# Optimization experiments

Hardware: AMD Instinct MI355X
Metric: run time of the kernel (lower is better)

## Reference

```python
import jax, jax.numpy as jnp
import numpy as np

EPS = 1e-8
LN_EPS = 1e-5
DIM, NHEADS = 512, 8
HEAD_DIM = DIM // NHEADS
SCALE = HEAD_DIM ** -0.5
ROLE_VOCAB = 8


def _layernorm(x, g, b):
    mu = x.mean(-1, keepdims=True)
    var = ((x - mu) ** 2).mean(-1, keepdims=True)
    return (x - mu) * jax.lax.rsqrt(var + LN_EPS) * g + b


def setup_inputs() -> dict:
    key = jax.random.key(0)
    ks = jax.random.split(key, 16)
    B, K, L, D = 8, 4, 1024, DIM
    s = 1.0 / np.sqrt(D)
    return {
        "state_repr": jax.random.normal(ks[0], (B, K, L, D), jnp.float32),
        "residue_mask": jax.random.randint(ks[1], (B, K, L), 0, 2) > 0,
        "state_weights": jax.random.uniform(ks[2], (B, K), jnp.float32),
        "state_roles": jax.random.randint(ks[3], (B, K), 0, ROLE_VOCAB),
        "state_present_mask": jnp.ones((B, K), dtype=bool),
        "role_emb": jax.random.normal(ks[4], (ROLE_VOCAB, D), jnp.float32),
        "Wq": jax.random.normal(ks[5], (D, D), jnp.float32) * s,
        "Wk": jax.random.normal(ks[6], (D, D), jnp.float32) * s,
        "Wv": jax.random.normal(ks[7], (D, D), jnp.float32) * s,
        "Wo": jax.random.normal(ks[8], (D, D), jnp.float32) * s,
        "ln1_g": jnp.ones((3 * D,), jnp.float32),
        "ln1_b": jnp.zeros((3 * D,), jnp.float32),
        "Wg1": jax.random.normal(ks[9], (D, 3 * D), jnp.float32) / np.sqrt(3 * D),
        "bg1": jnp.zeros((D,), jnp.float32),
        "Wg2": jax.random.normal(ks[10], (D, D), jnp.float32) * s,
        "bg2": jnp.zeros((D,), jnp.float32),
        "norm_g": jnp.ones((D,), jnp.float32),
        "norm_b": jnp.zeros((D,), jnp.float32),
    }


def _forward(state_repr, residue_mask, state_weights, state_roles, state_present_mask,
             role_emb, Wq, Wk, Wv, Wo, ln1_g, ln1_b, Wg1, bg1, Wg2, bg2, norm_g, norm_b):
    B, K, L, D = state_repr.shape
    H, hd = NHEADS, HEAD_DIM
    roles = jnp.maximum(state_roles, 0)
    role_e = role_emb[roles][:, :, None, :]                       # [B,K,1,D]
    valid = residue_mask & state_present_mask[:, :, None]          # [B,K,L]

    # normalized state weights
    pres = state_present_mask.astype(jnp.float32)
    w = state_weights.astype(jnp.float32) * pres
    denom = w.sum(1, keepdims=True)
    fallback = pres / jnp.maximum(pres.sum(1, keepdims=True), 1.0)
    nsw = jnp.where(denom > EPS, w / jnp.maximum(denom, EPS), fallback)  # [B,K]

    x = (state_repr + role_e) * valid[..., None]
    x = x.transpose(0, 2, 1, 3)                                    # [B,L,K,D]
    valid_rlk = valid.transpose(0, 2, 1)                           # [B,L,K]

    def proj(W):  # torch Linear: y = x @ W.T
        return (x @ W.T).reshape(B, L, K, H, hd).transpose(0, 1, 3, 2, 4)  # [B,L,H,K,hd]

    q, k, v = proj(Wq), proj(Wk), proj(Wv)
    logits = jnp.einsum('blhqd,blhkd->blhqk', q, k) * SCALE
    logits = logits + jnp.log(jnp.maximum(nsw, EPS))[:, None, None, None, :]
    key_mask = valid_rlk[:, :, None, None, :]                      # [B,L,1,1,K]
    logits = jnp.where(key_mask, logits, -jnp.inf)
    attn = jax.nn.softmax(logits, axis=-1)
    attn = jnp.nan_to_num(attn, nan=0.0, posinf=0.0, neginf=0.0)
    attn_out = jnp.einsum('blhqk,blhkd->blhqd', attn, v)
    attn_out = attn_out.transpose(0, 1, 3, 2, 4).reshape(B, L, K, D)
    attn_out = (attn_out @ Wo.T) * valid_rlk[..., None]

    swr = nsw[:, None, :] * valid_rlk.astype(jnp.float32)          # [B,L,K]
    swr = swr / jnp.maximum(swr.sum(-1, keepdims=True), EPS)
    weighted_mean = jnp.sum(x * swr[..., None], axis=2)            # [B,L,D]
    attn_pooled = jnp.sum(attn_out * swr[..., None], axis=2)

    max_in = jnp.where(valid_rlk[..., None], x, -1e9)
    max_feat = max_in.max(axis=2)
    has_any = valid_rlk.any(axis=2, keepdims=True)
    max_feat = jnp.where(has_any, max_feat, 0.0)

    fusion_base = 0.5 * (attn_pooled + weighted_mean)
    gate_in = jnp.concatenate([attn_pooled, weighted_mean, max_feat], axis=-1)
    h = _layernorm(gate_in, ln1_g, ln1_b)
    h = jax.nn.gelu(h @ Wg1.T + bg1, approximate=False)
    gate = jax.nn.sigmoid(h @ Wg2.T + bg2)
    fused = gate * fusion_base + (1.0 - gate) * max_feat
    fused = _layernorm(fused + weighted_mean, norm_g, norm_b)

    attn_mean = attn.mean(axis=(2, 3))                             # [B,L,K]
    return fused, attn_pooled, weighted_mean, max_feat, attn_mean, nsw


def reference(state_repr, residue_mask, state_weights, state_roles, state_present_mask,
              role_emb, Wq, Wk, Wv, Wo, ln1_g, ln1_b, Wg1, bg1, Wg2, bg2, norm_g, norm_b):
    return _forward(state_repr, residue_mask, state_weights, state_roles, state_present_mask,
                    role_emb, Wq, Wk, Wv, Wo, ln1_g, ln1_b, Wg1, bg1, Wg2, bg2, norm_g, norm_b)
```

## Files before the change

kernel.cpp:

```cpp
#include <hip/hip_runtime.h>
#include <math.h>

#define BB 8
#define KK 4
#define LL 1024
#define DD 512
#define HD 64
#define D3 1536
#define MM (BB*LL*KK)
#define BL (BB*LL)
#define SCALE 0.125f
#define EPSF 1e-8f
#define LN_EPSF 1e-5f

typedef _Float16 hfrag __attribute__((ext_vector_type(8)));
typedef float f32x4 __attribute__((ext_vector_type(4)));

__device__ __forceinline__ unsigned short f2h(float f) {
    _Float16 h = (_Float16)f;
    unsigned short u; __builtin_memcpy(&u, &h, 2); return u;
}
__device__ __forceinline__ float h2f(unsigned short u) {
    _Float16 h; __builtin_memcpy(&h, &u, 2); return (float)h;
}

__device__ __forceinline__ void glds16(const unsigned short* g, unsigned short* l) {
    __builtin_amdgcn_global_load_lds(
        (const __attribute__((address_space(1))) void*)g,
        (__attribute__((address_space(3))) void*)l, 16, 0, 0);
}

__device__ __forceinline__ void nsw_compute(const float* sw, const int* pres,
                                            int b, float* nswv) {
    float w[KK], pr[KK]; float denom = 0.f, ps = 0.f;
    #pragma unroll
    for (int k = 0; k < KK; ++k) {
        pr[k] = pres[b*KK + k] ? 1.f : 0.f;
        w[k]  = sw[b*KK + k] * pr[k];
        denom += w[k]; ps += pr[k];
    }
    #pragma unroll
    for (int k = 0; k < KK; ++k)
        nswv[k] = (denom > EPSF) ? w[k] / fmaxf(denom, EPSF)
                                 : pr[k] / fmaxf(ps, 1.f);
}

#define WSZ 262144
#define OG1 1048576
#define OG2 1835008
#define WTOT 2097152
__global__ __launch_bounds__(256) void cvt_weights(
        const float* __restrict__ Wq, const float* __restrict__ Wk,
        const float* __restrict__ Wv, const float* __restrict__ Wo,
        const float* __restrict__ Wg1, const float* __restrict__ Wg2,
        unsigned short* __restrict__ dst) {
    int t = blockIdx.x * 256 + threadIdx.x;
    int e = t * 4;
    const float* src; int off;
    if      (e < WSZ)    { src = Wq;  off = e; }
    else if (e < 2*WSZ)  { src = Wk;  off = e - WSZ; }
    else if (e < 3*WSZ)  { src = Wv;  off = e - 2*WSZ; }
    else if (e < OG1)    { src = Wo;  off = e - 3*WSZ; }
    else if (e < OG2)    { src = Wg1; off = e - OG1; }
    else                 { src = Wg2; off = e - OG2; }
    float4 v = *(const float4*)(src + off);
    ushort4 o;
    o.x = f2h(v.x); o.y = f2h(v.y); o.z = f2h(v.z); o.w = f2h(v.w);
    *(ushort4*)(dst + e) = o;
}

__global__ __launch_bounds__(256) void buildx_kernel(
        const float* __restrict__ SR, const int* __restrict__ residue,
        const int* __restrict__ pres, const int* __restrict__ roles,
        const float* __restrict__ role_emb, const float* __restrict__ sw,
        unsigned short* __restrict__ Xh, float* __restrict__ rowmask,
        float* __restrict__ out_wm, float* __restrict__ out_mx,
        float* __restrict__ f_nsw) {
    int t  = blockIdx.x * 256 + threadIdx.x;
    int bl = t >> 7;
    int d4 = (t & 127) << 2;
    int b  = bl >> 10, l = bl & 1023;
    float nswv[KK];
    nsw_compute(sw, pres, b, nswv);
    float mk[KK], swr[KK];
    float ssum = 0.f, many = 0.f;
    #pragma unroll
    for (int k = 0; k < KK; ++k) {
        int bk = b*KK + k;
        bool valid = (residue[(size_t)bk*LL + l] != 0) && (pres[bk] != 0);
        mk[k]  = valid ? 1.f : 0.f;
        swr[k] = nswv[k] * mk[k];
        ssum += swr[k]; many += mk[k];
    }
    float inv = 1.f / fmaxf(ssum, EPSF);
    bool hasany = many > 0.5f;
    float wmx = 0.f, wmy = 0.f, wmz = 0.f, wmw = 0.f;
    float mxx = -1e9f, mxy = -1e9f, mxz = -1e9f, mxw = -1e9f;
    #pragma unroll
    for (int k = 0; k < KK; ++k) {
        int bk = b*KK + k;
        int role = roles[bk]; if (role < 0) role = 0;
        float4 sr = *(const float4*)(SR + ((size_t)bk*LL + l)*DD + d4);
        float4 re = *(const float4*)(role_emb + (size_t)role*DD + d4);
        float xx = (sr.x + re.x)*mk[k], xy = (sr.y + re.y)*mk[k];
        float xz = (sr.z + re.z)*mk[k], xw = (sr.w + re.w)*mk[k];
        ushort4 xs; xs.x = f2h(xx); xs.y = f2h(xy); xs.z = f2h(xz); xs.w = f2h(xw);
        *(ushort4*)(Xh + (size_t)(bl*KK + k)*DD + d4) = xs;
        float s = swr[k]*inv;
        wmx = fmaf(xx, s, wmx); wmy = fmaf(xy, s, wmy);
        wmz = fmaf(xz, s, wmz); wmw = fmaf(xw, s, wmw);
        if (mk[k] > 0.5f) {
            mxx = fmaxf(mxx, xx); mxy = fmaxf(mxy, xy);
            mxz = fmaxf(mxz, xz); mxw = fmaxf(mxw, xw);
        }
    }
    if (!hasany) { mxx = mxy = mxz = mxw = 0.f; }
    float4 wmv; wmv.x = wmx; wmv.y = wmy; wmv.z = wmz; wmv.w = wmw;
    float4 mxv; mxv.x = mxx; mxv.y = mxy; mxv.z = mxz; mxv.w = mxw;
    *(float4*)(out_wm + (size_t)bl*DD + d4) = wmv;
    *(float4*)(out_mx + (size_t)bl*DD + d4) = mxv;
    if (d4 == 0) {
        #pragma unroll
        for (int k = 0; k < KK; ++k) rowmask[bl*KK + k] = mk[k];
    }
    if (blockIdx.x == 0 && threadIdx.x < BB*KK) {
        int bb = threadIdx.x >> 2, kk2 = threadIdx.x & 3;
        float nv[KK];
        nsw_compute(sw, pres, bb, nv);
        f_nsw[threadIdx.x] = nv[kk2];
    }
}

template<int TM, int EPI, int OUTH, int QKVR, int SWZ>
__global__ __launch_bounds__(256) void gemm_mfma(
        const unsigned short* __restrict__ A, const unsigned short* __restrict__ W,
        void* __restrict__ Cv, int M, int N, int Kd,
        const float* __restrict__ bias, const float* __restrict__ rowmask) {
    constexpr int FI = TM / 32;
    __shared__ __align__(16) unsigned short As[TM*32];
    __shared__ __align__(16) unsigned short Bs[128*32];
    const int tid  = threadIdx.x;
    const int wave = tid >> 6, lane = tid & 63;
    int m0, n0;
    if (SWZ) {
        int id = blockIdx.x;
        int c = id & 7, j = id >> 3;
        int mloc = j / 12;
        m0 = (c*32 + mloc) * TM;
        n0 = (j - mloc*12) * 128;
    } else {
        m0 = blockIdx.y * TM; n0 = blockIdx.x * 128;
    }
    const int srow = lane >> 2;
    const int scol = (lane & 3) << 3;
    const int arow = (TM == 128) ? (wave*32 + srow)
                   : (TM == 64)  ? (wave*16 + srow)
                   :               ((wave & 1)*16 + srow);
    const bool astage = (TM >= 64) || (wave < 2);
    const unsigned short* Ag0 = A + (size_t)(m0 + arow) * Kd + scol;
    const unsigned short* Ag1 = Ag0 + (size_t)16 * Kd;
    unsigned short* Al0 = As + arow*32 + scol;
    unsigned short* Al1 = Al0 + 16*32;
    const unsigned short* Wp0 = W + (size_t)(n0 + wave*32 + srow) * Kd + scol;
    const unsigned short* Wp1 = Wp0 + (size_t)16 * Kd;
    unsigned short* Bl0 = Bs + (wave*32 + srow)*32 + scol;
    unsigned short* Bl1 = Bl0 + 16*32;
    const int wr = (wave >> 1) * (TM/2);
    const int wc = (wave & 1) * 64;
    const int fr = lane & 15;
    const int fq = (lane >> 4) * 8;
    f32x4 acc[FI][4] = {};
    for (int k0 = 0; k0 < Kd; k0 += 32) {
        if (astage)    glds16(Ag0 + k0, Al0);
        if (TM == 128) glds16(Ag1 + k0, Al1);
        glds16(Wp0 + k0, Bl0);
        glds16(Wp1 + k0, Bl1);
        __syncthreads();
        hfrag af[FI], bf[4];
        #pragma unroll
        for (int i = 0; i < FI; ++i)
            af[i] = *(const hfrag*)(As + (wr + i*16 + fr)*32 + fq);
        #pragma unroll
        for (int j = 0; j < 4; ++j)
            bf[j] = *(const hfrag*)(Bs + (wc + j*16 + fr)*32 + fq);
        #pragma unroll
        for (int i = 0; i < FI; ++i)
            #pragma unroll
            for (int j = 0; j < 4; ++j)
                acc[i][j] = __builtin_amdgcn_mfma_f32_16x16x32_f16(af[i], bf[j], acc[i][j], 0, 0, 0);
        __syncthreads();
    }
    unsigned short* Ch = (unsigned short*)Cv;
    int Nout = N, colbase = n0;
    if (QKVR) {
        const int seg = n0 >> 9;
        Ch = (unsigned short*)Cv + (size_t)seg * M * 512;
        Nout = 512;
        colbase = n0 - (seg << 9);
    }
    #pragma unroll
    for (int i = 0; i < FI; ++i) {
        const int row = m0 + wr + i*16 + (lane >> 4)*4;
        #pragma unroll
        for (int j = 0; j < 4; ++j) {
            const int col = colbase + wc + j*16 + (lane & 15);
            float bv = (EPI == 2) ? bias[col] : 0.f;
            #pragma unroll
            for (int r = 0; r < 4; ++r) {
                float v = acc[i][j][r];
                if (EPI == 2) { v += bv; v = 0.5f * v * (1.f + erff(v * 0.70710678118654752f)); }
                if (OUTH) Ch[(size_t)(row + r) * Nout + col] = f2h(v);
                else      ((float*)Cv)[(size_t)(row + r) * Nout + col] = v;
            }
        }
    }
}

__global__ __launch_bounds__(512, 4) void gemm_qkv_8p(
        const unsigned short* __restrict__ A, const unsigned short* __restrict__ W,
        unsigned short* __restrict__ Cbase) {
    __shared__ __align__(16) unsigned short smem[36864];
    const int tid  = threadIdx.x;
    const int wave = tid >> 6, lane = tid & 63;
    const int id = blockIdx.x;
    const int wg = (id & 7) * 192 + (id >> 3);
    const int m0 = (wg / 12) * 256;
    const int n0 = (wg % 12) * 128;
    const int wm = wave >> 1, wn = wave & 1;
    const int fr = lane & 15, q = lane >> 4;
    const int srow = tid >> 2, scc = tid & 3;
    const int sswz = (scc ^ ((srow >> 1) & 3)) << 3;
    const unsigned short* Ag0 = A + (size_t)(m0 + srow)*512 + sswz;
    const unsigned short* Ag1 = Ag0 + (size_t)128*512;
    const unsigned short* Wg0 = W + (size_t)(n0 + srow)*512 + sswz;
    const int lA0 = tid << 3;
    const int lA1 = (tid + 512) << 3;
    int aoff[4], boff[4];
    #pragma unroll
    for (int mf = 0; mf < 4; ++mf) {
        int row = (wm << 6) + (mf << 4) + fr;
        aoff[mf] = (row << 5) + ((q ^ ((row >> 1) & 3)) << 3);
    }
    #pragma unroll
    for (int nf = 0; nf < 4; ++nf) {
        int row = (wn << 6) + (nf << 4) + fr;
        boff[nf] = (row << 5) + ((q ^ ((row >> 1) & 3)) << 3);
    }
    f32x4 acc[4][4] = {};

#define VMWAIT(N) asm volatile("s_waitcnt vmcnt(" #N ")" ::: "memory")
#define STAGE(tt) do { unsigned short* _d = smem + ((tt) % 3) * 12288; \
        const int _ko = (tt) << 5; \
        glds16(Ag0 + _ko, _d + lA0); glds16(Ag1 + _ko, _d + lA1); \
        glds16(Wg0 + _ko, _d + 8192 + lA0); } while (0)
#define MFROW(ai, areg) \
        acc[ai][0] = __builtin_amdgcn_mfma_f32_16x16x32_f16(areg, b0, acc[ai][0], 0, 0, 0); \
        acc[ai][1] = __builtin_amdgcn_mfma_f32_16x16x32_f16(areg, b1, acc[ai][1], 0, 0, 0); \
        acc[ai][2] = __builtin_amdgcn_mfma_f32_16x16x32_f16(areg, b2, acc[ai][2], 0, 0, 0); \
        acc[ai][3] = __builtin_amdgcn_mfma_f32_16x16x32_f16(areg, b3, acc[ai][3], 0, 0, 0);
#define TILE(t, STG, VM) do { \
        const unsigned short* _Ab = smem + ((t) % 3) * 12288; \
        const unsigned short* _Bb = _Ab + 8192; \
        VMWAIT(VM); \
        __builtin_amdgcn_s_barrier(); \
        __builtin_amdgcn_sched_barrier(0); \
        hfrag b0 = *(const hfrag*)(_Bb + boff[0]); \
        hfrag b1 = *(const hfrag*)(_Bb + boff[1]); \
        hfrag b2 = *(const hfrag*)(_Bb + boff[2]); \
        hfrag b3 = *(const hfrag*)(_Bb + boff[3]); \
        hfrag a0_ = *(const hfrag*)(_Ab + aoff[0]); \
        hfrag a1_ = *(const hfrag*)(_Ab + aoff[1]); \
        hfrag a2_ = *(const hfrag*)(_Ab + aoff[2]); \
        hfrag a3_ = *(const hfrag*)(_Ab + aoff[3]); \
        if (STG) STAGE((t) + 2); \
        __builtin_amdgcn_s_setprio(1); \
        MFROW(0, a0_) MFROW(1, a1_) MFROW(2, a2_) MFROW(3, a3_) \
        __builtin_amdgcn_s_setprio(0); \
    } while (0)

    STAGE(0); STAGE(1);
    #pragma unroll
    for (int t = 0; t < 14; ++t) TILE(t, 1, 3);
    TILE(14, 0, 3);
    TILE(15, 0, 0);
#undef TILE
#undef MFROW
#undef STAGE
#undef VMWAIT

    const int gc0 = n0 + (wn << 6);
    const int seg = gc0 >> 9;
    unsigned short* Cs = Cbase + (size_t)seg * ((size_t)MM * 512);
    const int cb = gc0 & 511;
    #pragma unroll
    for (int mf = 0; mf < 4; ++mf) {
        const int grow = m0 + (wm << 6) + (mf << 4) + (q << 2);
        #pragma unroll
        for (int nf = 0; nf < 4; ++nf) {
            const int col = cb + (nf << 4) + fr;
            #pragma unroll
            for (int r = 0; r < 4; ++r)
                Cs[(size_t)(grow + r) * 512 + col] = f2h(acc[mf][nf][r]);
        }
    }
}

__global__ __launch_bounds__(256) void wo_pool_kernel(
        const unsigned short* __restrict__ A,
        const unsigned short* __restrict__ W,
        const float* __restrict__ sw, const int* __restrict__ pres,
        const float* __restrict__ rmask,
        const float* __restrict__ in_wm, const float* __restrict__ in_mx,
        const float* __restrict__ ln1_g, const float* __restrict__ ln1_b,
        float* __restrict__ out_ap, unsigned short* __restrict__ hin) {
    __shared__ __align__(16) unsigned short As[32*32];
    __shared__ __align__(16) unsigned short Bs[512*32];
    const int tid = threadIdx.x, wave = tid >> 6, lane = tid & 63;
    const int m0 = blockIdx.x * 32;
    const int srow = lane >> 2, scol = (lane & 3) << 3;
    const unsigned short* Ag = A + (size_t)(m0 + wave*16 + srow)*512 + scol;
    unsigned short* Al = As + (wave*16 + srow)*32 + scol;
    const int brow = wave*128 + srow;
    const unsigned short* Wg = W + (size_t)brow*512 + scol;
    unsigned short* Blb = Bs + brow*32 + scol;
    const int q = lane >> 4, frl = lane & 15;
    const int fq = q * 8;
    f32x4 acc[2][8] = {};
    for (int k0 = 0; k0 < 512; k0 += 32) {
        if (wave < 2) glds16(Ag + k0, Al);
        #pragma unroll
        for (int i = 0; i < 8; ++i)
            glds16(Wg + (size_t)i*16*512 + k0, Blb + i*16*32);
        __syncthreads();
        hfrag af[2], bf[8];
        #pragma unroll
        for (int i = 0; i < 2; ++i)
            af[i] = *(const hfrag*)(As + (i*16 + frl)*32 + fq);
        #pragma unroll
        for (int j = 0; j < 8; ++j)
            bf[j] = *(const hfrag*)(Bs + (wave*128 + j*16 + frl)*32 + fq);
        #pragma unroll
        for (int i = 0; i < 2; ++i)
            #pragma unroll
            for (int j = 0; j < 8; ++j)
                acc[i][j] = __builtin_amdgcn_mfma_f32_16x16x32_f16(af[i], bf[j], acc[i][j], 0, 0, 0);
        __syncthreads();
    }
    float* ap_s = (float*)Bs;
    const int bl0 = m0 >> 2;
    const int b = bl0 >> 10;
    float nv[KK];
    nsw_compute(sw, pres, b, nv);
    #pragma unroll
    for (int i = 0; i < 2; ++i) {
        int bl_loc = i*4 + q;
        int blg = bl0 + bl_loc;
        float s4[KK]; float ssum = 0.f;
        #pragma unroll
        for (int k = 0; k < KK; ++k) { s4[k] = nv[k] * rmask[blg*4 + k]; ssum += s4[k]; }
        float inv = 1.f / fmaxf(ssum, EPSF);
        #pragma unroll
        for (int j = 0; j < 8; ++j) {
            float ap = 0.f;
            #pragma unroll
            for (int r = 0; r < KK; ++r) ap = fmaf(s4[r]*inv, acc[i][j][r], ap);
            ap_s[bl_loc*512 + wave*128 + j*16 + frl] = ap;
        }
    }
    __syncthreads();
    const int blq = tid >> 5;
    const int c0  = (tid & 31) * 16;
    const int blg = bl0 + blq;
    float4 ap4[4], wm4[4], mx4[4];
    #pragma unroll
    for (int v = 0; v < 4; ++v) {
        ap4[v] = *(const float4*)(ap_s + blq*512 + c0 + v*4);
        wm4[v] = *(const float4*)(in_wm + (size_t)blg*512 + c0 + v*4);
        mx4[v] = *(const float4*)(in_mx + (size_t)blg*512 + c0 + v*4);
    }
    float s = 0.f, s2 = 0.f;
    #pragma unroll
    for (int c = 0; c < 16; ++c) {
        float ap = ((const float*)ap4)[c];
        float wm = ((const float*)wm4)[c];
        float mx = ((const float*)mx4)[c];
        s += ap + wm + mx; s2 += ap*ap + wm*wm + mx*mx;
    }
    #pragma unroll
    for (int o = 1; o < 32; o <<= 1) {
        s  += __shfl_xor(s,  o, 32);
        s2 += __shfl_xor(s2, o, 32);
    }
    float mu = s * (1.f/(float)D3);
    float var = s2 * (1.f/(float)D3) - mu*mu;
    float rstd = rsqrtf(var + LN_EPSF);
    #pragma unroll
    for (int v = 0; v < 4; ++v)
        *(float4*)(out_ap + (size_t)blg*512 + c0 + v*4) = ap4[v];
    #pragma unroll
    for (int seg = 0; seg < 3; ++seg) {
        const float* src = (seg == 0) ? (const float*)ap4
                         : (seg == 1) ? (const float*)wm4 : (const float*)mx4;
        int gofs = seg*512 + c0;
        #pragma unroll
        for (int v = 0; v < 4; ++v) {
            float4 g4 = *(const float4*)(ln1_g + gofs + v*4);
            float4 b4 = *(const float4*)(ln1_b + gofs + v*4);
            ushort4 o;
            o.x = f2h((src[v*4+0]-mu)*rstd*g4.x + b4.x);
            o.y = f2h((src[v*4+1]-mu)*rstd*g4.y + b4.y);
            o.z = f2h((src[v*4+2]-mu)*rstd*g4.z + b4.z);
            o.w = f2h((src[v*4+3]-mu)*rstd*g4.w + b4.w);
            *(ushort4*)(hin + (size_t)blg*D3 + gofs + v*4) = o;
        }
    }
}

__global__ __launch_bounds__(256) void wg2_final_kernel(
        const unsigned short* __restrict__ A,
        const unsigned short* __restrict__ W,
        const float* __restrict__ bg2,
        const float* __restrict__ in_ap, const float* __restrict__ in_wm,
        const float* __restrict__ in_mx,
        const float* __restrict__ norm_g, const float* __restrict__ norm_b,
        float* __restrict__ fused) {
    __shared__ __align__(16) unsigned short As[16*32];
    __shared__ __align__(16) unsigned short Bs[512*32];
    __shared__ float rs[16*4], rq[16*4];
    const int tid = threadIdx.x, wave = tid >> 6, lane = tid & 63;
    const int m0 = blockIdx.x * 16;
    const int srow = lane >> 2, scol = (lane & 3) << 3;
    const unsigned short* Ag = A + (size_t)(m0 + srow)*512 + scol;
    unsigned short* Al = As + srow*32 + scol;
    const int brow = wave*128 + srow;
    const unsigned short* Wg = W + (size_t)brow*512 + scol;
    unsigned short* Blb = Bs + brow*32 + scol;
    const int q = lane >> 4, frl = lane & 15;
    const int fq = q * 8;
    f32x4 acc[8] = {};
    for (int k0 = 0; k0 < 512; k0 += 32) {
        if (wave == 0) glds16(Ag + k0, Al);
        #pragma unroll
        for (int i = 0; i < 8; ++i)
            glds16(Wg + (size_t)i*16*512 + k0, Blb + i*16*32);
        __syncthreads();
        hfrag af, bf[8];
        af = *(const hfrag*)(As + frl*32 + fq);
        #pragma unroll
        for (int j = 0; j < 8; ++j)
            bf[j] = *(const hfrag*)(Bs + (wave*128 + j*16 + frl)*32 + fq);
        #pragma unroll
        for (int j = 0; j < 8; ++j)
            acc[j] = __builtin_amdgcn_mfma_f32_16x16x32_f16(af, bf[j], acc[j], 0, 0, 0);
        __syncthreads();
    }
    float pre[8][4];
    float s[4] = {}, s2[4] = {};
    #pragma unroll
    for (int j = 0; j < 8; ++j) {
        int col = wave*128 + j*16 + frl;
        float bv = bg2[col];
        #pragma unroll
        for (int r = 0; r < 4; ++r) {
            int row = m0 + q*4 + r;
            float g = 1.f / (1.f + expf(-(acc[j][r] + bv)));
            float ap = in_ap[(size_t)row*512 + col];
            float wm = in_wm[(size_t)row*512 + col];
            float mx = in_mx[(size_t)row*512 + col];
            float p = g*0.5f*(ap + wm) + (1.f - g)*mx + wm;
            pre[j][r] = p;
            s[r] += p; s2[r] += p*p;
        }
    }
    #pragma unroll
    for (int r = 0; r < 4; ++r) {
        #pragma unroll
        for (int o = 1; o < 16; o <<= 1) {
            s[r]  += __shfl_xor(s[r],  o, 64);
            s2[r] += __shfl_xor(s2[r], o, 64);
        }
        if (frl == 0) {
            rs[(q*4+r)*4 + wave] = s[r];
            rq[(q*4+r)*4 + wave] = s2[r];
        }
    }
    __syncthreads();
    float mu[4], rstd[4];
    #pragma unroll
    for (int r = 0; r < 4; ++r) {
        int rl = q*4 + r;
        float ts  = rs[rl*4] + rs[rl*4+1] + rs[rl*4+2] + rs[rl*4+3];
        float tq  = rq[rl*4] + rq[rl*4+1] + rq[rl*4+2] + rq[rl*4+3];
        float m = ts * (1.f/(float)DD);
        float v = tq * (1.f/(float)DD) - m*m;
        mu[r] = m; rstd[r] = rsqrtf(v + LN_EPSF);
    }
    #pragma unroll
    for (int j = 0; j < 8; ++j) {
        int col = wave*128 + j*16 + frl;
        float g = norm_g[col], bb = norm_b[col];
        #pragma unroll
        for (int r = 0; r < 4; ++r) {
            int row = m0 + q*4 + r;
            fused[(size_t)row*512 + col] = (pre[j][r]-mu[r])*rstd[r]*g + bb;
        }
    }
}

__global__ __launch_bounds__(256) void attn_kernel(
        unsigned short* Qb ,
        const unsigned short* __restrict__ Kb, const unsigned short* __restrict__ Vb,
        const float* __restrict__ sw, const int* __restrict__ pres,
        const float* __restrict__ rowmask,
        float* __restrict__ attn_mean_out) {
    __shared__ float qs[KK][DD];
    __shared__ float ksm[KK][DD];
    __shared__ float vs[KK][DD];
    __shared__ float att[128];
    __shared__ float lw[KK], mk[KK];
    int bl = blockIdx.x, b = bl >> 10, mb = bl * KK;
    int tid = threadIdx.x;
    const ushort4* q4 = (const ushort4*)(Qb + (size_t)mb*DD);
    const ushort4* k4 = (const ushort4*)(Kb + (size_t)mb*DD);
    const ushort4* v4 = (const ushort4*)(Vb + (size_t)mb*DD);
    #pragma unroll
    for (int p = 0; p < 2; ++p) {
        int idx = p*256 + tid;
        int k = idx >> 7, dd = (idx & 127) << 2;
        ushort4 a = q4[idx];
        qs[k][dd] = h2f(a.x); qs[k][dd+1] = h2f(a.y); qs[k][dd+2] = h2f(a.z); qs[k][dd+3] = h2f(a.w);
        ushort4 c = k4[idx];
        ksm[k][dd] = h2f(c.x); ksm[k][dd+1] = h2f(c.y); ksm[k][dd+2] = h2f(c.z); ksm[k][dd+3] = h2f(c.w);
        ushort4 e = v4[idx];
        vs[k][dd] = h2f(e.x); vs[k][dd+1] = h2f(e.y); vs[k][dd+2] = h2f(e.z); vs[k][dd+3] = h2f(e.w);
    }
    if (tid < KK) {
        float nv[KK];
        nsw_compute(sw, pres, b, nv);
        lw[tid] = logf(fmaxf(nv[tid], EPSF));
        mk[tid] = rowmask[mb + tid];
    }
    __syncthreads();
    if (tid < 128) {
        int h = tid >> 4, i = (tid >> 2) & 3, j = tid & 3;
        float s = 0.f;
        #pragma unroll 16
        for (int d = 0; d < HD; ++d) s = fmaf(qs[i][h*HD + d], ksm[j][h*HD + d], s);
        float lg = s * SCALE + lw[j];
        att[tid] = (mk[j] > 0.5f) ? lg : -INFINITY;
    }
    __syncthreads();
    if (tid < 32) {
        int base = tid * 4;
        float l0 = att[base], l1 = att[base+1], l2 = att[base+2], l3 = att[base+3];
        float m = fmaxf(fmaxf(l0, l1), fmaxf(l2, l3));
        if (m == -INFINITY) {
            att[base] = att[base+1] = att[base+2] = att[base+3] = 0.f;
        } else {
            float e0 = expf(l0 - m), e1 = expf(l1 - m), e2 = expf(l2 - m), e3 = expf(l3 - m);
            float inv = 1.f / (e0 + e1 + e2 + e3);
            att[base] = e0*inv; att[base+1] = e1*inv; att[base+2] = e2*inv; att[base+3] = e3*inv;
        }
    }
    __syncthreads();
    if (tid < KK) {
        float s = 0.f;
        for (int hi = 0; hi < 32; ++hi) s += att[hi*4 + tid];
        attn_mean_out[(size_t)bl*KK + tid] = s * (1.f/32.f);
    }
    float outv[8];
    #pragma unroll
    for (int p = 0; p < 8; ++p) {
        int idx = p*256 + tid;
        int i = idx >> 9, dc = idx & 511, h = dc >> 6;
        float s = 0.f;
        #pragma unroll
        for (int j = 0; j < KK; ++j) s = fmaf(att[h*16 + i*4 + j], vs[j][dc], s);
        outv[p] = s;
    }
    #pragma unroll
    for (int p = 0; p < 8; ++p) {
        int idx = p*256 + tid;
        int i = idx >> 9, dc = idx & 511;
        Qb[(size_t)(mb+i)*DD + dc] = f2h(outv[p]);
    }
}

extern "C" void kernel_launch(void* const* d_in, const int* in_sizes, int n_in,
                              void* d_out, int out_size, void* d_ws, size_t ws_size,
                              hipStream_t stream) {
    const float* SR      = (const float*)d_in[0];
    const int*   residue = (const int*)d_in[1];
    const float* sw      = (const float*)d_in[2];
    const int*   roles   = (const int*)d_in[3];
    const int*   pres    = (const int*)d_in[4];
    const float* role_emb= (const float*)d_in[5];
    const float* Wq      = (const float*)d_in[6];
    const float* Wk      = (const float*)d_in[7];
    const float* Wv      = (const float*)d_in[8];
    const float* Wo      = (const float*)d_in[9];
    const float* ln1_g   = (const float*)d_in[10];
    const float* ln1_b   = (const float*)d_in[11];
    const float* Wg1     = (const float*)d_in[12];
    const float* bg1     = (const float*)d_in[13];
    const float* Wg2     = (const float*)d_in[14];
    const float* bg2     = (const float*)d_in[15];
    const float* norm_g  = (const float*)d_in[16];
    const float* norm_b  = (const float*)d_in[17];

    float* out = (float*)d_out;
    const size_t BLD = (size_t)BL * DD;
    float* f_fused = out;
    float* f_ap    = out + BLD;
    float* f_wm    = out + 2*BLD;
    float* f_mx    = out + 3*BLD;
    float* f_am    = out + 4*BLD;
    float* f_nsw   = out + 4*BLD + (size_t)BL*KK;

    char* base = (char*)d_ws;
    const size_t MD2 = (size_t)MM * DD * 2;
    unsigned short* Xh = (unsigned short*)(base);
    unsigned short* Qh = (unsigned short*)(base + MD2);
    unsigned short* Kh = (unsigned short*)(base + 2*MD2);
    unsigned short* Vh = (unsigned short*)(base + 3*MD2);
    unsigned short* Wb = (unsigned short*)(base + 4*MD2);
    float* rmask = (float*)(base + 4*MD2 + (size_t)WTOT*2);
    unsigned short* AOh  = Qh;
    unsigned short* Hin  = Vh;
    unsigned short* Hbuf = Xh;
    const unsigned short* Wqkv = Wb;
    const unsigned short* Woh  = Wb + 3*WSZ;
    const unsigned short* Wg1h = Wb + OG1;
    const unsigned short* Wg2h = Wb + OG2;

    dim3 blk(256);

    cvt_weights<<<WTOT/1024, blk, 0, stream>>>(Wq, Wk, Wv, Wo, Wg1, Wg2, Wb);
    buildx_kernel<<<(BL*128)/256, blk, 0, stream>>>(SR, residue, pres, roles, role_emb,
                                                    sw, Xh, rmask, f_wm, f_mx, f_nsw);

    gemm_qkv_8p<<<dim3(1536), dim3(512), 0, stream>>>(Xh, Wqkv, Qh);

    attn_kernel<<<BL, blk, 0, stream>>>(Qh, Kh, Vh, sw, pres, rmask, f_am);

    wo_pool_kernel<<<dim3(MM/32), blk, 0, stream>>>(
        AOh, Woh, sw, pres, rmask, f_wm, f_mx, ln1_g, ln1_b, f_ap, Hin);

    gemm_mfma<32,2,1,0,0><<<dim3(4, BL/32), blk, 0, stream>>>(
        Hin, Wg1h, Hbuf, BL, DD, D3, bg1, nullptr);

    wg2_final_kernel<<<dim3(BL/16), blk, 0, stream>>>(
        Hbuf, Wg2h, bg2, f_ap, f_wm, f_mx, norm_g, norm_b, f_fused);
}
```

Baseline: 375.2 us.

## Replace gate GEMM with triple-buffered swizzled MFMA kernel; stream attention from global

Swaps the generic 32-row gate-1 GEMM for a dedicated 128x128-tile kernel. It uses triple-buffered async global-to-LDS staging, XOR-swizzled LDS layout, explicit vmcnt waits and priority hints, with the bias+GELU epilogue fused in. Separately, the attention kernel drops its LDS staging of Q/K/V in fp32. It now reads Q/K as 16-byte half vectors directly from global memory for the scores and V as half2 pairs for the output, which removes LDS traffic and occupancy pressure. The GEMM change trades tile size and grid width (256 blocks) for better reuse and latency hiding. The attention change relies on cache hits for repeated global reads.

Result: faster. 353.7 us (-5.7%).

```diff
diff --git a/kernel.cpp b/kernel.cpp
--- a/kernel.cpp
+++ b/kernel.cpp
@@ -128,91 +128,6 @@
         float nv[KK];
         nsw_compute(sw, pres, bb, nv);
         f_nsw[threadIdx.x] = nv[kk2];
-    }
-}
-
-template<int TM, int EPI, int OUTH, int QKVR, int SWZ>
-__global__ __launch_bounds__(256) void gemm_mfma(
-        const unsigned short* __restrict__ A, const unsigned short* __restrict__ W,
-        void* __restrict__ Cv, int M, int N, int Kd,
-        const float* __restrict__ bias, const float* __restrict__ rowmask) {
-    constexpr int FI = TM / 32;
-    __shared__ __align__(16) unsigned short As[TM*32];
-    __shared__ __align__(16) unsigned short Bs[128*32];
-    const int tid  = threadIdx.x;
-    const int wave = tid >> 6, lane = tid & 63;
-    int m0, n0;
-    if (SWZ) {
-        int id = blockIdx.x;
-        int c = id & 7, j = id >> 3;
-        int mloc = j / 12;
-        m0 = (c*32 + mloc) * TM;
-        n0 = (j - mloc*12) * 128;
-    } else {
-        m0 = blockIdx.y * TM; n0 = blockIdx.x * 128;
-    }
-    const int srow = lane >> 2;
-    const int scol = (lane & 3) << 3;
-    const int arow = (TM == 128) ? (wave*32 + srow)
-                   : (TM == 64)  ? (wave*16 + srow)
-                   :               ((wave & 1)*16 + srow);
-    const bool astage = (TM >= 64) || (wave < 2);
-    const unsigned short* Ag0 = A + (size_t)(m0 + arow) * Kd + scol;
-    const unsigned short* Ag1 = Ag0 + (size_t)16 * Kd;
-    unsigned short* Al0 = As + arow*32 + scol;
-    unsigned short* Al1 = Al0 + 16*32;
-    const unsigned short* Wp0 = W + (size_t)(n0 + wave*32 + srow) * Kd + scol;
-    const unsigned short* Wp1 = Wp0 + (size_t)16 * Kd;
-    unsigned short* Bl0 = Bs + (wave*32 + srow)*32 + scol;
-    unsigned short* Bl1 = Bl0 + 16*32;
-    const int wr = (wave >> 1) * (TM/2);
-    const int wc = (wave & 1) * 64;
-    const int fr = lane & 15;
-    const int fq = (lane >> 4) * 8;
-    f32x4 acc[FI][4] = {};
-    for (int k0 = 0; k0 < Kd; k0 += 32) {
-        if (astage)    glds16(Ag0 + k0, Al0);
-        if (TM == 128) glds16(Ag1 + k0, Al1);
-        glds16(Wp0 + k0, Bl0);
-        glds16(Wp1 + k0, Bl1);
-        __syncthreads();
-        hfrag af[FI], bf[4];
-        #pragma unroll
-        for (int i = 0; i < FI; ++i)
-            af[i] = *(const hfrag*)(As + (wr + i*16 + fr)*32 + fq);
-        #pragma unroll
-        for (int j = 0; j < 4; ++j)
-            bf[j] = *(const hfrag*)(Bs + (wc + j*16 + fr)*32 + fq);
-        #pragma unroll
-        for (int i = 0; i < FI; ++i)
-            #pragma unroll
-            for (int j = 0; j < 4; ++j)
-                acc[i][j] = __builtin_amdgcn_mfma_f32_16x16x32_f16(af[i], bf[j], acc[i][j], 0, 0, 0);
-        __syncthreads();
-    }
-    unsigned short* Ch = (unsigned short*)Cv;
-    int Nout = N, colbase = n0;
-    if (QKVR) {
-        const int seg = n0 >> 9;
-        Ch = (unsigned short*)Cv + (size_t)seg * M * 512;
-        Nout = 512;
-        colbase = n0 - (seg << 9);
-    }
-    #pragma unroll
-    for (int i = 0; i < FI; ++i) {
-        const int row = m0 + wr + i*16 + (lane >> 4)*4;
-        #pragma unroll
-        for (int j = 0; j < 4; ++j) {
-            const int col = colbase + wc + j*16 + (lane & 15);
-            float bv = (EPI == 2) ? bias[col] : 0.f;
-            #pragma unroll
-            for (int r = 0; r < 4; ++r) {
-                float v = acc[i][j][r];
-                if (EPI == 2) { v += bv; v = 0.5f * v * (1.f + erff(v * 0.70710678118654752f)); }
-                if (OUTH) Ch[(size_t)(row + r) * Nout + col] = f2h(v);
-                else      ((float*)Cv)[(size_t)(row + r) * Nout + col] = v;
-            }
-        }
     }
 }
 
@@ -305,6 +220,96 @@
     }
 }
 
+__global__ __launch_bounds__(256, 3) void gemm_g1(
+        const unsigned short* __restrict__ A, const unsigned short* __restrict__ W,
+        unsigned short* __restrict__ C, const float* __restrict__ bias) {
+    __shared__ __align__(16) unsigned short smem[24576];
+    const int tid  = threadIdx.x;
+    const int wave = tid >> 6, lane = tid & 63;
+    const int id = blockIdx.x;
+    const int wg = (id & 7) * 32 + (id >> 3);
+    const int m0 = (wg >> 2) * 128;
+    const int n0 = (wg & 3) * 128;
+    const int wm = wave >> 1, wn = wave & 1;
+    const int fr = lane & 15, q = lane >> 4;
+    const int srow = tid >> 2, scc = tid & 3;
+    const int sswz = (scc ^ ((srow >> 1) & 3)) << 3;
+    const unsigned short* Ag0 = A + (size_t)(m0 + srow)*D3 + sswz;
+    const unsigned short* Ag1 = Ag0 + (size_t)64*D3;
+    const unsigned short* Wg0 = W + (size_t)(n0 + srow)*D3 + sswz;
+    const unsigned short* Wg1p = Wg0 + (size_t)64*D3;
+    const int lA0 = tid << 3;
+    const int lA1 = (tid + 256) << 3;
+    int aoff[4], boff[4];
+    #pragma unroll
+    for (int mf = 0; mf < 4; ++mf) {
+        int row = (wm << 6) + (mf << 4) + fr;
+        aoff[mf] = (row << 5) + ((q ^ ((row >> 1) & 3)) << 3);
+    }
+    #pragma unroll
+    for (int nf = 0; nf < 4; ++nf) {
+        int row = (wn << 6) + (nf << 4) + fr;
+        boff[nf] = (row << 5) + ((q ^ ((row >> 1) & 3)) << 3);
+    }
+    f32x4 acc[4][4] = {};
+
+#define VMWAIT(N) asm volatile("s_waitcnt vmcnt(" #N ")" ::: "memory")
+#define STAGE(tt) do { unsigned short* _d = smem + ((tt) % 3) * 8192; \
+        const int _ko = (tt) << 5; \
+        glds16(Ag0 + _ko, _d + lA0); glds16(Ag1 + _ko, _d + lA1); \
+        glds16(Wg0 + _ko, _d + 4096 + lA0); glds16(Wg1p + _ko, _d + 4096 + lA1); } while (0)
+#define MFROW(ai, areg) \
+        acc[ai][0] = __builtin_amdgcn_mfma_f32_16x16x32_f16(areg, b0, acc[ai][0], 0, 0, 0); \
+        acc[ai][1] = __builtin_amdgcn_mfma_f32_16x16x32_f16(areg, b1, acc[ai][1], 0, 0, 0); \
+        acc[ai][2] = __builtin_amdgcn_mfma_f32_16x16x32_f16(areg, b2, acc[ai][2], 0, 0, 0); \
+        acc[ai][3] = __builtin_amdgcn_mfma_f32_16x16x32_f16(areg, b3, acc[ai][3], 0, 0, 0);
+#define TILE(t, STG, VM) do { \
+        const unsigned short* _Ab = smem + ((t) % 3) * 8192; \
+        const unsigned short* _Bb = _Ab + 4096; \
+        VMWAIT(VM); \
+        __builtin_amdgcn_s_barrier(); \
+        __builtin_amdgcn_sched_barrier(0); \
+        hfrag b0 = *(const hfrag*)(_Bb + boff[0]); \
+        hfrag b1 = *(const hfrag*)(_Bb + boff[1]); \
+        hfrag b2 = *(const hfrag*)(_Bb + boff[2]); \
+        hfrag b3 = *(const hfrag*)(_Bb + boff[3]); \
+        hfrag a0_ = *(const hfrag*)(_Ab + aoff[0]); \
+        hfrag a1_ = *(const hfrag*)(_Ab + aoff[1]); \
+        hfrag a2_ = *(const hfrag*)(_Ab + aoff[2]); \
+        hfrag a3_ = *(const hfrag*)(_Ab + aoff[3]); \
+        if (STG) STAGE((t) + 2); \
+        __builtin_amdgcn_s_setprio(1); \
+        MFROW(0, a0_) MFROW(1, a1_) MFROW(2, a2_) MFROW(3, a3_) \
+        __builtin_amdgcn_s_setprio(0); \
+    } while (0)
+
+    STAGE(0); STAGE(1);
+    #pragma unroll 3
+    for (int t = 0; t < 46; ++t) TILE(t, 1, 4);
+    TILE(46, 0, 4);
+    TILE(47, 0, 0);
+#undef TILE
+#undef MFROW
+#undef STAGE
+#undef VMWAIT
+
+    #pragma unroll
+    for (int mf = 0; mf < 4; ++mf) {
+        const int grow = m0 + (wm << 6) + (mf << 4) + (q << 2);
+        #pragma unroll
+        for (int nf = 0; nf < 4; ++nf) {
+            const int col = n0 + (wn << 6) + (nf << 4) + fr;
+            const float bv = bias[col];
+            #pragma unroll
+            for (int r = 0; r < 4; ++r) {
+                float v = acc[mf][nf][r] + bv;
+                v = 0.5f * v * (1.f + erff(v * 0.70710678118654752f));
+                C[(size_t)(grow + r) * 512 + col] = f2h(v);
+            }
+        }
+    }
+}
+
 __global__ __launch_bounds__(256) void wo_pool_kernel(
         const unsigned short* __restrict__ A,
         const unsigned short* __restrict__ W,
@@ -513,27 +518,10 @@
         const float* __restrict__ sw, const int* __restrict__ pres,
         const float* __restrict__ rowmask,
         float* __restrict__ attn_mean_out) {
-    __shared__ float qs[KK][DD];
-    __shared__ float ksm[KK][DD];
-    __shared__ float vs[KK][DD];
     __shared__ float att[128];
     __shared__ float lw[KK], mk[KK];
     int bl = blockIdx.x, b = bl >> 10, mb = bl * KK;
     int tid = threadIdx.x;
-    const ushort4* q4 = (const ushort4*)(Qb + (size_t)mb*DD);
-    const ushort4* k4 = (const ushort4*)(Kb + (size_t)mb*DD);
-    const ushort4* v4 = (const ushort4*)(Vb + (size_t)mb*DD);
-    #pragma unroll
-    for (int p = 0; p < 2; ++p) {
-        int idx = p*256 + tid;
-        int k = idx >> 7, dd = (idx & 127) << 2;
-        ushort4 a = q4[idx];
-        qs[k][dd] = h2f(a.x); qs[k][dd+1] = h2f(a.y); qs[k][dd+2] = h2f(a.z); qs[k][dd+3] = h2f(a.w);
-        ushort4 c = k4[idx];
-        ksm[k][dd] = h2f(c.x); ksm[k][dd+1] = h2f(c.y); ksm[k][dd+2] = h2f(c.z); ksm[k][dd+3] = h2f(c.w);
-        ushort4 e = v4[idx];
-        vs[k][dd] = h2f(e.x); vs[k][dd+1] = h2f(e.y); vs[k][dd+2] = h2f(e.z); vs[k][dd+3] = h2f(e.w);
-    }
     if (tid < KK) {
         float nv[KK];
         nsw_compute(sw, pres, b, nv);
@@ -543,9 +531,17 @@
     __syncthreads();
     if (tid < 128) {
         int h = tid >> 4, i = (tid >> 2) & 3, j = tid & 3;
+        const unsigned short* qp = Qb + (size_t)(mb + i)*DD + h*HD;
+        const unsigned short* kp = Kb + (size_t)(mb + j)*DD + h*HD;
         float s = 0.f;
-        #pragma unroll 16
-        for (int d = 0; d < HD; ++d) s = fmaf(qs[i][h*HD + d], ksm[j][h*HD + d], s);
+        #pragma unroll
+        for (int c = 0; c < 8; ++c) {
+            hfrag qv = *(const hfrag*)(qp + c*8);
+            hfrag kv = *(const hfrag*)(kp + c*8);
+            #pragma unroll
+            for (int e = 0; e < 8; ++e)
+                s = fmaf((float)qv[e], (float)kv[e], s);
+        }
         float lg = s * SCALE + lw[j];
         att[tid] = (mk[j] > 0.5f) ? lg : -INFINITY;
     }
@@ -568,21 +564,20 @@
         for (int hi = 0; hi < 32; ++hi) s += att[hi*4 + tid];
         attn_mean_out[(size_t)bl*KK + tid] = s * (1.f/32.f);
     }
-    float outv[8];
-    #pragma unroll
-    for (int p = 0; p < 8; ++p) {
+    #pragma unroll
+    for (int p = 0; p < 4; ++p) {
         int idx = p*256 + tid;
-        int i = idx >> 9, dc = idx & 511, h = dc >> 6;
-        float s = 0.f;
-        #pragma unroll
-        for (int j = 0; j < KK; ++j) s = fmaf(att[h*16 + i*4 + j], vs[j][dc], s);
-        outv[p] = s;
-    }
-    #pragma unroll
-    for (int p = 0; p < 8; ++p) {
-        int idx = p*256 + tid;
-        int i = idx >> 9, dc = idx & 511;
-        Qb[(size_t)(mb+i)*DD + dc] = f2h(outv[p]);
+        int i = idx >> 8, d2 = (idx & 255) << 1, h = d2 >> 6;
+        float s0 = 0.f, s1 = 0.f;
+        #pragma unroll
+        for (int j = 0; j < KK; ++j) {
+            float aj = att[h*16 + i*4 + j];
+            ushort2 vv = *(const ushort2*)(Vb + (size_t)(mb + j)*DD + d2);
+            s0 = fmaf(aj, h2f(vv.x), s0);
+            s1 = fmaf(aj, h2f(vv.y), s1);
+        }
+        ushort2 o; o.x = f2h(s0); o.y = f2h(s1);
+        *(ushort2*)(Qb + (size_t)(mb + i)*DD + d2) = o;
     }
 }
 
@@ -646,8 +641,7 @@
     wo_pool_kernel<<<dim3(MM/32), blk, 0, stream>>>(
         AOh, Woh, sw, pres, rmask, f_wm, f_mx, ln1_g, ln1_b, f_ap, Hin);
 
-    gemm_mfma<32,2,1,0,0><<<dim3(4, BL/32), blk, 0, stream>>>(
-        Hin, Wg1h, Hbuf, BL, DD, D3, bg1, nullptr);
+    gemm_g1<<<dim3(256), blk, 0, stream>>>(Hin, Wg1h, Hbuf, bg1);
 
     wg2_final_kernel<<<dim3(BL/16), blk, 0, stream>>>(
         Hbuf, Wg2h, bg2, f_ap, f_wm, f_mx, norm_g, norm_b, f_fused);
```
